# Optimization experiments

Hardware: AMD Instinct MI355X
Metric: run time of the kernel (lower is better)

## Reference

```python
import jax, jax.numpy as jnp
import numpy as np


def _knn(coords, k):
    # coords: [N, 3]. Returns indices of the k nearest neighbors (self excluded): [N, k]
    sq = jnp.sum(coords * coords, axis=1)
    d2 = sq[:, None] + sq[None, :] - 2.0 * (coords @ coords.T)  # [N, N]
    n = coords.shape[0]
    d2 = jnp.where(jnp.eye(n, dtype=bool), jnp.inf, d2)  # loop=False: no self edges
    _, idx = jax.lax.top_k(-d2, k)
    return idx


def setup_inputs() -> dict:
    key = jax.random.key(0)
    ks = jax.random.split(key, 7)
    B, N, C = 8, 4096, 6
    feats = jax.random.normal(ks[0], (B, N, C), dtype=jnp.float32)
    # Glorot-ish scaled weights; PyG GCNConv lin has no bias, bias added post-aggregation.
    W1 = jax.random.normal(ks[1], (6, 64), dtype=jnp.float32) * (1.0 / np.sqrt(6))
    b1 = jnp.zeros((64,), dtype=jnp.float32)
    W2 = jax.random.normal(ks[2], (64, 128), dtype=jnp.float32) * (1.0 / np.sqrt(64))
    b2 = jnp.zeros((128,), dtype=jnp.float32)
    Wf = jax.random.normal(ks[3], (128, 128), dtype=jnp.float32) * (1.0 / np.sqrt(128))
    bf = jnp.zeros((128,), dtype=jnp.float32)
    return {"feats": feats, "W1": W1, "b1": b1, "W2": W2, "b2": b2,
            "Wf": Wf, "bf": bf, "k": 16}


def reference(feats, W1, b1, W2, b2, Wf, bf, k):
    # feats: [B, N, C]; coords = first 3 channels.
    coords = feats[..., :3]
    nbr = jax.vmap(lambda c: _knn(c, k))(coords)  # [B, N, k]
    inv_deg = 1.0 / (k + 1)  # every node has exactly k in-edges + self loop (uniform sym norm)
    x = feats
    for W, b in ((W1, b1), (W2, b2)):
        h = x @ W  # [B, N, H]
        nb = jax.vmap(lambda hb, ib: hb[ib])(h, nbr)  # gather neighbor feats: [B, N, k, H]
        x = jax.nn.relu((nb.sum(axis=2) + h) * inv_deg + b)  # GCN aggregate + bias + ReLU
    return x @ Wf + bf  # [B, N, out_dim]
```

## Files before the change

### kernel.cpp

```cpp
#include <hip/hip_runtime.h>
#include <cstdint>
#include <cstddef>

#define NPTS 4096
#define KNN  16
#define INV_DEG (1.0f / 17.0f)
#define CAP  48
#define TS   512

typedef unsigned long long u64;
typedef unsigned int u32;
typedef float v2f __attribute__((ext_vector_type(2)));

__device__ __forceinline__ u32 mapmono(float f) {
  u32 u = __float_as_uint(f);
  return u ^ ((u32)((int)u >> 31) | 0x80000000u);
}
__device__ __forceinline__ float unmapmono(u32 m) {
  u32 u = (m & 0x80000000u) ? (m ^ 0x80000000u) : ~m;
  return __uint_as_float(u);
}

__global__ __launch_bounds__(512) void knn_kernel(const float* __restrict__ feats,
                                                  int* __restrict__ nbr) {
#pragma clang fp contract(off)
  __shared__ float4 sc[TS];
  __shared__ u64 sbuf[8][2][64];

  const int b = blockIdx.x >> 8;
  const int pbase = (blockIdx.x & 255) * 16;
  const float* fb = feats + (size_t)b * NPTS * 6;
  const int wave = threadIdx.x >> 6;
  const int lane = threadIdx.x & 63;

  int ip[2];
  float xi[2], yi[2], zi[2], sqi[2], tau[2];
  u64 slot[2];
  int cnt[2];
#pragma unroll
  for (int p = 0; p < 2; ++p) {
    ip[p] = pbase + wave * 2 + p;
    const float* fr = fb + (size_t)ip[p] * 6;
    xi[p] = fr[0]; yi[p] = fr[1]; zi[p] = fr[2];
    sqi[p] = __fadd_rn(__fadd_rn(__fmul_rn(xi[p], xi[p]), __fmul_rn(yi[p], yi[p])),
                       __fmul_rn(zi[p], zi[p]));
    tau[p] = __uint_as_float(0x7f800000u);
    slot[p] = ~0ull;
    cnt[p] = 0;
  }

  auto flush = [&](int p, bool fin) {
    u64* wb = &sbuf[wave][p][0];
    if (lane >= cnt[p] && lane < CAP) wb[lane] = ~0ull;
    if (lane < KNN) wb[CAP + lane] = slot[p];
    u64 myk = wb[lane];
    if ((u32)myk == (u32)ip[p]) {
      myk = ~0ull;
      wb[lane] = ~0ull;
    }
    int rank = 0;
#pragma unroll
    for (int m = 0; m < 64; m += 4) {
      u64 k0 = wb[m], k1 = wb[m + 1], k2 = wb[m + 2], k3 = wb[m + 3];
      rank += (int)(k0 < myk) + (int)(k1 < myk) + (int)(k2 < myk) + (int)(k3 < myk);
    }
    if (fin) {
      if (rank < KNN)
        nbr[((size_t)(b * NPTS) + ip[p]) * KNN + rank] = (int)(u32)myk;
    } else {
      if (rank < KNN) wb[rank] = myk;
      u64 s15 = wb[15];
      if (lane < KNN) slot[p] = wb[lane];
      tau[p] = unmapmono((u32)(s15 >> 32));
    }
    cnt[p] = 0;
  };

  for (int tb = 0; tb < NPTS; tb += TS) {
    __syncthreads();
    for (int t = threadIdx.x; t < TS; t += 512) {
      const float* fr = fb + (size_t)(tb + t) * 6;
      const float x = fr[0], y = fr[1], z = fr[2];
      const float sq = __fadd_rn(__fadd_rn(__fmul_rn(x, x), __fmul_rn(y, y)),
                                 __fmul_rn(z, z));
      float4 c; c.x = x; c.y = y; c.z = z; c.w = sq;
      sc[t] = c;
    }
    __syncthreads();

    for (int jb0 = 0; jb0 < TS; jb0 += 64) {
      const int tl = jb0 + lane;
      const int j = tb + tl;
      const float4 c = sc[tl];
      const v2f cx2 = {c.x, c.x}, cy2 = {c.y, c.y}, cz2 = {c.z, c.z},
                sq2 = {c.w, c.w};
      v2f X = {xi[0], xi[1]};
      v2f Y = {yi[0], yi[1]};
      v2f Z = {zi[0], zi[1]};
      v2f SQ = {sqi[0], sqi[1]};
      v2f dot = X * cx2;
      dot = __builtin_elementwise_fma(Y, cy2, dot);
      dot = __builtin_elementwise_fma(Z, cz2, dot);
      v2f two = {2.0f, 2.0f};
      v2f d2v = (SQ + sq2) - two * dot;
      float d2s[2] = {d2v.x, d2v.y};
#pragma unroll
      for (int p = 0; p < 2; ++p) {
        const bool pred = d2s[p] <= tau[p];
        const u64 bal = __ballot(pred);
        if (bal) {
          const int npass = __popcll(bal);
          if (cnt[p] + npass > CAP) flush(p, false);
          const int pos = cnt[p] + (int)__builtin_amdgcn_mbcnt_hi(
                                        (u32)(bal >> 32),
                                        __builtin_amdgcn_mbcnt_lo((u32)bal, 0));
          const u64 key = ((u64)mapmono(d2s[p]) << 32) | (u32)j;
          if (npass <= CAP) {
            if (pred) sbuf[wave][p][pos] = key;
            cnt[p] += npass;
          } else {
            if (pred && pos < CAP) sbuf[wave][p][pos] = key;
            cnt[p] = CAP;
            flush(p, false);
            if (pred && pos >= CAP) sbuf[wave][p][pos - CAP] = key;
            cnt[p] = npass - CAP;
          }
        }
      }
    }
  }
#pragma unroll
  for (int p = 0; p < 2; ++p) flush(p, true);
}

__global__ __launch_bounds__(256) void enc1_kernel(const float* __restrict__ feats,
                                                   const int* __restrict__ nbr,
                                                   const float* __restrict__ W1,
                                                   const float* __restrict__ b1,
                                                   float* __restrict__ x1) {
  __shared__ float af[64][6];
  const int tid = threadIdx.x;
  const int n0 = blockIdx.x * 64;
  const int gb = n0 & ~(NPTS - 1);

  if (tid < 128) {
    const int p = tid >> 1, h = tid & 1;
    const int n = n0 + p;
    const int d0 = h * 3;
    const int* nb = nbr + (size_t)n * KNN;
    const float* fr = feats + (size_t)n * 6 + d0;
    float a0 = fr[0], a1 = fr[1], a2 = fr[2];
#pragma unroll
    for (int t = 0; t < KNN; ++t) {
      const float* fq = feats + (size_t)(gb + nb[t]) * 6 + d0;
      a0 += fq[0]; a1 += fq[1]; a2 += fq[2];
    }
    af[p][d0] = a0; af[p][d0 + 1] = a1; af[p][d0 + 2] = a2;
  }
  __syncthreads();

  const int c = tid & 63, pg = tid >> 6;
  float w[6];
#pragma unroll
  for (int k = 0; k < 6; ++k) w[k] = W1[k * 64 + c];
  const float bv = b1[c];
  for (int pi = 0; pi < 16; ++pi) {
    const int p = pg * 16 + pi;
    float s = 0.f;
#pragma unroll
    for (int k = 0; k < 6; ++k) s = fmaf(af[p][k], w[k], s);
    x1[(size_t)(n0 + p) * 64 + c] = fmaxf(fmaf(s, INV_DEG, bv), 0.f);
  }
}

__global__ __launch_bounds__(256) void enc2_kernel(const float* __restrict__ x1,
                                                   const int* __restrict__ nbr,
                                                   const float* __restrict__ W2,
                                                   const float* __restrict__ b2,
                                                   float* __restrict__ x2) {
  __shared__ float a1s[16][64];
  __shared__ v2f w2s[64][64];
  const int tid = threadIdx.x;
  const int n0 = blockIdx.x * 16;
  const int gb = n0 & ~(NPTS - 1);

#pragma unroll
  for (int i = 0; i < 16; ++i) {
    const int e = tid + 256 * i;
    const int k = e >> 6, l = e & 63;
    v2f w;
    w.x = W2[k * 128 + l];
    w.y = W2[k * 128 + 64 + l];
    w2s[k][l] = w;
  }
  {
    const int p = tid >> 4, c4 = tid & 15;
    const int n = n0 + p;
    const int* nb = nbr + (size_t)n * KNN;
    float4 s = ((const float4*)(x1 + (size_t)n * 64))[c4];
#pragma unroll
    for (int t = 0; t < KNN; ++t) {
      float4 v = ((const float4*)(x1 + (size_t)(gb + nb[t]) * 64))[c4];
      s.x += v.x; s.y += v.y; s.z += v.z; s.w += v.w;
    }
    *((float4*)&a1s[p][c4 * 4]) = s;
  }
  __syncthreads();

  const int wave = tid >> 6, lane = tid & 63;
  const int p0 = wave * 4;
  const float bx = b2[lane], by = b2[lane + 64];
  v2f acc0 = {0, 0}, acc1 = {0, 0}, acc2 = {0, 0}, acc3 = {0, 0};
  for (int k = 0; k < 64; k += 4) {
    const float4 a0 = *(const float4*)&a1s[p0 + 0][k];
    const float4 a1v = *(const float4*)&a1s[p0 + 1][k];
    const float4 a2v = *(const float4*)&a1s[p0 + 2][k];
    const float4 a3v = *(const float4*)&a1s[p0 + 3][k];
#pragma unroll
    for (int kk = 0; kk < 4; ++kk) {
      const v2f w = w2s[k + kk][lane];
      const float e0 = kk == 0 ? a0.x : kk == 1 ? a0.y : kk == 2 ? a0.z : a0.w;
      const float e1 = kk == 0 ? a1v.x : kk == 1 ? a1v.y : kk == 2 ? a1v.z : a1v.w;
      const float e2 = kk == 0 ? a2v.x : kk == 1 ? a2v.y : kk == 2 ? a2v.z : a2v.w;
      const float e3 = kk == 0 ? a3v.x : kk == 1 ? a3v.y : kk == 2 ? a3v.z : a3v.w;
      v2f v0 = {e0, e0}, v1 = {e1, e1}, v2 = {e2, e2}, v3 = {e3, e3};
      acc0 = __builtin_elementwise_fma(v0, w, acc0);
      acc1 = __builtin_elementwise_fma(v1, w, acc1);
      acc2 = __builtin_elementwise_fma(v2, w, acc2);
      acc3 = __builtin_elementwise_fma(v3, w, acc3);
    }
  }
  v2f accs[4] = {acc0, acc1, acc2, acc3};
#pragma unroll
  for (int pi = 0; pi < 4; ++pi) {
    float* row = x2 + (size_t)(n0 + p0 + pi) * 128;
    row[lane] = fmaxf(fmaf(accs[pi].x, INV_DEG, bx), 0.f);
    row[lane + 64] = fmaxf(fmaf(accs[pi].y, INV_DEG, by), 0.f);
  }
}

__global__ __launch_bounds__(256) void enc3_kernel(const float* __restrict__ x2,
                                                   const float* __restrict__ Wf,
                                                   const float* __restrict__ bf,
                                                   float* __restrict__ out) {
  __shared__ float xs[16 * 128];
  __shared__ float part[2][16][128];
  const int tid = threadIdx.x;
  const int n0 = blockIdx.x * 16;

#pragma unroll
  for (int i = 0; i < 2; ++i) {
    const int e = tid + 256 * i;
    ((float4*)xs)[e] = ((const float4*)(x2 + (size_t)n0 * 128))[e];
  }

  const int wave = tid >> 6, lane = tid & 63;
  const int kh = wave & 1, pg = wave >> 1;
  v2f w[64];
#pragma unroll
  for (int j = 0; j < 64; ++j) {
    const int k = kh * 64 + j;
    w[j].x = Wf[k * 128 + lane];
    w[j].y = Wf[k * 128 + 64 + lane];
  }
  __syncthreads();

  for (int pi = 0; pi < 8; ++pi) {
    const int p = pg * 8 + pi;
    v2f acc = {0, 0};
    for (int j = 0; j < 64; j += 4) {
      const float4 a = *(const float4*)&xs[p * 128 + kh * 64 + j];
#pragma unroll
      for (int jj = 0; jj < 4; ++jj) {
        const float e = jj == 0 ? a.x : jj == 1 ? a.y : jj == 2 ? a.z : a.w;
        v2f v = {e, e};
        acc = __builtin_elementwise_fma(v, w[j + jj], acc);
      }
    }
    part[kh][p][lane] = acc.x;
    part[kh][p][lane + 64] = acc.y;
  }
  __syncthreads();

#pragma unroll
  for (int i = 0; i < 8; ++i) {
    const int e = tid + 256 * i;
    const int p = e >> 7, c = e & 127;
    out[(size_t)(n0 + p) * 128 + c] = part[0][p][c] + part[1][p][c] + bf[c];
  }
}

extern "C" void kernel_launch(void* const* d_in, const int* in_sizes, int n_in,
                              void* d_out, int out_size, void* d_ws, size_t ws_size,
                              hipStream_t stream) {
  const float* feats = (const float*)d_in[0];
  const float* W1 = (const float*)d_in[1];
  const float* b1 = (const float*)d_in[2];
  const float* W2 = (const float*)d_in[3];
  const float* b2 = (const float*)d_in[4];
  const float* Wf = (const float*)d_in[5];
  const float* bf = (const float*)d_in[6];
  float* out = (float*)d_out;

  char* ws = (char*)d_ws;
  int* nbr = (int*)ws;
  float* x1 = (float*)(ws + (size_t)(2 << 20));
  float* x2 = out;

  knn_kernel<<<2048, 512, 0, stream>>>(feats, nbr);
  enc1_kernel<<<512, 256, 0, stream>>>(feats, nbr, W1, b1, x1);
  enc2_kernel<<<2048, 256, 0, stream>>>(x1, nbr, W2, b2, x2);
  enc3_kernel<<<2048, 256, 0, stream>>>(x2, Wf, bf, out);
}
```

Baseline: 233.6 us.

## Fuse first GCN layer into KNN kernel and defer key mapping to flush

The first GCN aggregation and its small matmul move into the tail of the KNN kernel. Each wave gathers its 16 neighbours plus itself from the final sorted slot list, sums them in shared memory and writes x1 directly, so the separate enc1 launch and its re-read of nbr go away. The monotone float-to-key mapping and the self-exclusion check leave the per-candidate hot loop and run only at flush time, using a raw-bit sentinel. enc2 and enc3 now process 32 points per block instead of 16, which halves their grids and gives enc2 more accumulators per wave, at the cost of more registers and shared memory.

```diff
diff --git a/kernel.cpp b/kernel.cpp
--- a/kernel.cpp
+++ b/kernel.cpp
@@ -12,17 +12,18 @@
 typedef unsigned int u32;
 typedef float v2f __attribute__((ext_vector_type(2)));
 
-__device__ __forceinline__ u32 mapmono(float f) {
-  u32 u = __float_as_uint(f);
-  return u ^ ((u32)((int)u >> 31) | 0x80000000u);
-}
+#define RAWSENT 0x7F800000FFFFFFFFull
+
 __device__ __forceinline__ float unmapmono(u32 m) {
   u32 u = (m & 0x80000000u) ? (m ^ 0x80000000u) : ~m;
   return __uint_as_float(u);
 }
 
 __global__ __launch_bounds__(512) void knn_kernel(const float* __restrict__ feats,
-                                                  int* __restrict__ nbr) {
+                                                  const float* __restrict__ W1,
+                                                  const float* __restrict__ b1,
+                                                  int* __restrict__ nbr,
+                                                  float* __restrict__ x1) {
 #pragma clang fp contract(off)
   __shared__ float4 sc[TS];
   __shared__ u64 sbuf[8][2][64];
@@ -49,14 +50,17 @@
     cnt[p] = 0;
   }
 
-  auto flush = [&](int p, bool fin) {
+  auto flush = [&](int p) {
     u64* wb = &sbuf[wave][p][0];
-    if (lane >= cnt[p] && lane < CAP) wb[lane] = ~0ull;
+    if (lane >= cnt[p] && lane < CAP) wb[lane] = RAWSENT;
     if (lane < KNN) wb[CAP + lane] = slot[p];
     u64 myk = wb[lane];
-    if ((u32)myk == (u32)ip[p]) {
-      myk = ~0ull;
-      wb[lane] = ~0ull;
+    if (lane < CAP) {
+      u32 hi = (u32)(myk >> 32);
+      hi ^= ((u32)((int)hi >> 31) | 0x80000000u);
+      myk = ((u64)hi << 32) | (u32)myk;
+      if ((u32)myk == (u32)ip[p]) myk = ~0ull;
+      wb[lane] = myk;
     }
     int rank = 0;
 #pragma unroll
@@ -64,15 +68,10 @@
       u64 k0 = wb[m], k1 = wb[m + 1], k2 = wb[m + 2], k3 = wb[m + 3];
       rank += (int)(k0 < myk) + (int)(k1 < myk) + (int)(k2 < myk) + (int)(k3 < myk);
     }
-    if (fin) {
-      if (rank < KNN)
-        nbr[((size_t)(b * NPTS) + ip[p]) * KNN + rank] = (int)(u32)myk;
-    } else {
-      if (rank < KNN) wb[rank] = myk;
-      u64 s15 = wb[15];
-      if (lane < KNN) slot[p] = wb[lane];
-      tau[p] = unmapmono((u32)(s15 >> 32));
-    }
+    if (rank < KNN) wb[rank] = myk;
+    u64 s15 = wb[15];
+    if (lane < KNN) slot[p] = wb[lane];
+    tau[p] = unmapmono((u32)(s15 >> 32));
     cnt[p] = 0;
   };
 
@@ -110,18 +109,18 @@
         const u64 bal = __ballot(pred);
         if (bal) {
           const int npass = __popcll(bal);
-          if (cnt[p] + npass > CAP) flush(p, false);
+          if (cnt[p] + npass > CAP) flush(p);
           const int pos = cnt[p] + (int)__builtin_amdgcn_mbcnt_hi(
                                         (u32)(bal >> 32),
                                         __builtin_amdgcn_mbcnt_lo((u32)bal, 0));
-          const u64 key = ((u64)mapmono(d2s[p]) << 32) | (u32)j;
+          const u64 key = ((u64)__float_as_uint(d2s[p]) << 32) | (u32)j;
           if (npass <= CAP) {
             if (pred) sbuf[wave][p][pos] = key;
             cnt[p] += npass;
           } else {
             if (pred && pos < CAP) sbuf[wave][p][pos] = key;
             cnt[p] = CAP;
-            flush(p, false);
+            flush(p);
             if (pred && pos >= CAP) sbuf[wave][p][pos - CAP] = key;
             cnt[p] = npass - CAP;
           }
@@ -130,46 +129,42 @@
     }
   }
 #pragma unroll
-  for (int p = 0; p < 2; ++p) flush(p, true);
-}
-
-__global__ __launch_bounds__(256) void enc1_kernel(const float* __restrict__ feats,
-                                                   const int* __restrict__ nbr,
-                                                   const float* __restrict__ W1,
-                                                   const float* __restrict__ b1,
-                                                   float* __restrict__ x1) {
-  __shared__ float af[64][6];
-  const int tid = threadIdx.x;
-  const int n0 = blockIdx.x * 64;
-  const int gb = n0 & ~(NPTS - 1);
-
-  if (tid < 128) {
-    const int p = tid >> 1, h = tid & 1;
-    const int n = n0 + p;
-    const int d0 = h * 3;
-    const int* nb = nbr + (size_t)n * KNN;
-    const float* fr = feats + (size_t)n * 6 + d0;
-    float a0 = fr[0], a1 = fr[1], a2 = fr[2];
-#pragma unroll
-    for (int t = 0; t < KNN; ++t) {
-      const float* fq = feats + (size_t)(gb + nb[t]) * 6 + d0;
-      a0 += fq[0]; a1 += fq[1]; a2 += fq[2];
-    }
-    af[p][d0] = a0; af[p][d0 + 1] = a1; af[p][d0 + 2] = a2;
-  }
-  __syncthreads();
-
-  const int c = tid & 63, pg = tid >> 6;
-  float w[6];
-#pragma unroll
-  for (int k = 0; k < 6; ++k) w[k] = W1[k * 64 + c];
-  const float bv = b1[c];
-  for (int pi = 0; pi < 16; ++pi) {
-    const int p = pg * 16 + pi;
+  for (int p = 0; p < 2; ++p) flush(p);
+
+  float* fsc = (float*)&sbuf[wave][0][0];
+  float w1r[6];
+#pragma unroll
+  for (int k = 0; k < 6; ++k) w1r[k] = W1[k * 64 + lane];
+  const float b1r = b1[lane];
+
+#pragma unroll
+  for (int p = 0; p < 2; ++p) {
+    const int n = b * NPTS + ip[p];
+    const int row = (lane < KNN) ? (int)(u32)slot[p] : ip[p];
+    if (lane < KNN)
+      nbr[(size_t)n * KNN + lane] = row;
+    if (lane < 17) {
+      const float* fr = fb + (size_t)row * 6;
+      float2 r0 = *(const float2*)(fr);
+      float2 r1 = *(const float2*)(fr + 2);
+      float2 r2 = *(const float2*)(fr + 4);
+      fsc[lane * 6 + 0] = r0.x; fsc[lane * 6 + 1] = r0.y;
+      fsc[lane * 6 + 2] = r1.x; fsc[lane * 6 + 3] = r1.y;
+      fsc[lane * 6 + 4] = r2.x; fsc[lane * 6 + 5] = r2.y;
+    }
+    __syncthreads();
+    if (lane < 6) {
+      float s = 0.f;
+#pragma unroll
+      for (int t = 0; t < 17; ++t) s += fsc[t * 6 + lane];
+      fsc[102 + lane] = s;
+    }
+    __syncthreads();
     float s = 0.f;
 #pragma unroll
-    for (int k = 0; k < 6; ++k) s = fmaf(af[p][k], w[k], s);
-    x1[(size_t)(n0 + p) * 64 + c] = fmaxf(fmaf(s, INV_DEG, bv), 0.f);
+    for (int k = 0; k < 6; ++k) s = fmaf(fsc[102 + k], w1r[k], s);
+    x1[(size_t)n * 64 + lane] = fmaxf(fmaf(s, INV_DEG, b1r), 0.f);
+    __syncthreads();
   }
 }
 
@@ -178,10 +173,10 @@
                                                    const float* __restrict__ W2,
                                                    const float* __restrict__ b2,
                                                    float* __restrict__ x2) {
-  __shared__ float a1s[16][64];
+  __shared__ float a1s[32][64];
   __shared__ v2f w2s[64][64];
   const int tid = threadIdx.x;
-  const int n0 = blockIdx.x * 16;
+  const int n0 = blockIdx.x * 32;
   const int gb = n0 & ~(NPTS - 1);
 
 #pragma unroll
@@ -193,8 +188,9 @@
     w.y = W2[k * 128 + 64 + l];
     w2s[k][l] = w;
   }
-  {
-    const int p = tid >> 4, c4 = tid & 15;
+#pragma unroll
+  for (int r = 0; r < 2; ++r) {
+    const int p = r * 16 + (tid >> 4), c4 = tid & 15;
     const int n = n0 + p;
     const int* nb = nbr + (size_t)n * KNN;
     float4 s = ((const float4*)(x1 + (size_t)n * 64))[c4];
@@ -208,34 +204,32 @@
   __syncthreads();
 
   const int wave = tid >> 6, lane = tid & 63;
-  const int p0 = wave * 4;
+  const int p0 = wave * 8;
   const float bx = b2[lane], by = b2[lane + 64];
-  v2f acc0 = {0, 0}, acc1 = {0, 0}, acc2 = {0, 0}, acc3 = {0, 0};
+  v2f acc[8];
+#pragma unroll
+  for (int i = 0; i < 8; ++i) acc[i] = (v2f){0, 0};
   for (int k = 0; k < 64; k += 4) {
-    const float4 a0 = *(const float4*)&a1s[p0 + 0][k];
-    const float4 a1v = *(const float4*)&a1s[p0 + 1][k];
-    const float4 a2v = *(const float4*)&a1s[p0 + 2][k];
-    const float4 a3v = *(const float4*)&a1s[p0 + 3][k];
+    float4 a[8];
+#pragma unroll
+    for (int i = 0; i < 8; ++i) a[i] = *(const float4*)&a1s[p0 + i][k];
 #pragma unroll
     for (int kk = 0; kk < 4; ++kk) {
       const v2f w = w2s[k + kk][lane];
-      const float e0 = kk == 0 ? a0.x : kk == 1 ? a0.y : kk == 2 ? a0.z : a0.w;
-      const float e1 = kk == 0 ? a1v.x : kk == 1 ? a1v.y : kk == 2 ? a1v.z : a1v.w;
-      const float e2 = kk == 0 ? a2v.x : kk == 1 ? a2v.y : kk == 2 ? a2v.z : a2v.w;
-      const float e3 = kk == 0 ? a3v.x : kk == 1 ? a3v.y : kk == 2 ? a3v.z : a3v.w;
-      v2f v0 = {e0, e0}, v1 = {e1, e1}, v2 = {e2, e2}, v3 = {e3, e3};
-      acc0 = __builtin_elementwise_fma(v0, w, acc0);
-      acc1 = __builtin_elementwise_fma(v1, w, acc1);
-      acc2 = __builtin_elementwise_fma(v2, w, acc2);
-      acc3 = __builtin_elementwise_fma(v3, w, acc3);
-    }
-  }
-  v2f accs[4] = {acc0, acc1, acc2, acc3};
-#pragma unroll
-  for (int pi = 0; pi < 4; ++pi) {
+#pragma unroll
+      for (int i = 0; i < 8; ++i) {
+        const float e = kk == 0 ? a[i].x : kk == 1 ? a[i].y : kk == 2 ? a[i].z
+                                                                      : a[i].w;
+        v2f v = {e, e};
+        acc[i] = __builtin_elementwise_fma(v, w, acc[i]);
+      }
+    }
+  }
+#pragma unroll
+  for (int pi = 0; pi < 8; ++pi) {
     float* row = x2 + (size_t)(n0 + p0 + pi) * 128;
-    row[lane] = fmaxf(fmaf(accs[pi].x, INV_DEG, bx), 0.f);
-    row[lane + 64] = fmaxf(fmaf(accs[pi].y, INV_DEG, by), 0.f);
+    row[lane] = fmaxf(fmaf(acc[pi].x, INV_DEG, bx), 0.f);
+    row[lane + 64] = fmaxf(fmaf(acc[pi].y, INV_DEG, by), 0.f);
   }
 }
 
@@ -243,13 +237,13 @@
                                                    const float* __restrict__ Wf,
                                                    const float* __restrict__ bf,
                                                    float* __restrict__ out) {
-  __shared__ float xs[16 * 128];
-  __shared__ float part[2][16][128];
+  __shared__ float xs[32 * 128];
+  __shared__ float part[2][32][128];
   const int tid = threadIdx.x;
-  const int n0 = blockIdx.x * 16;
-
-#pragma unroll
-  for (int i = 0; i < 2; ++i) {
+  const int n0 = blockIdx.x * 32;
+
+#pragma unroll
+  for (int i = 0; i < 4; ++i) {
     const int e = tid + 256 * i;
     ((float4*)xs)[e] = ((const float4*)(x2 + (size_t)n0 * 128))[e];
   }
@@ -265,8 +259,8 @@
   }
   __syncthreads();
 
-  for (int pi = 0; pi < 8; ++pi) {
-    const int p = pg * 8 + pi;
+  for (int pi = 0; pi < 16; ++pi) {
+    const int p = pg * 16 + pi;
     v2f acc = {0, 0};
     for (int j = 0; j < 64; j += 4) {
       const float4 a = *(const float4*)&xs[p * 128 + kh * 64 + j];
@@ -283,7 +277,7 @@
   __syncthreads();
 
 #pragma unroll
-  for (int i = 0; i < 8; ++i) {
+  for (int i = 0; i < 16; ++i) {
     const int e = tid + 256 * i;
     const int p = e >> 7, c = e & 127;
     out[(size_t)(n0 + p) * 128 + c] = part[0][p][c] + part[1][p][c] + bf[c];
@@ -307,8 +301,7 @@
   float* x1 = (float*)(ws + (size_t)(2 << 20));
   float* x2 = out;
 
-  knn_kernel<<<2048, 512, 0, stream>>>(feats, nbr);
-  enc1_kernel<<<512, 256, 0, stream>>>(feats, nbr, W1, b1, x1);
-  enc2_kernel<<<2048, 256, 0, stream>>>(x1, nbr, W2, b2, x2);
-  enc3_kernel<<<2048, 256, 0, stream>>>(x2, Wf, bf, out);
-}
+  knn_kernel<<<2048, 512, 0, stream>>>(feats, W1, b1, nbr, x1);
+  enc2_kernel<<<1024, 256, 0, stream>>>(x1, nbr, W2, b2, x2);
+  enc3_kernel<<<1024, 256, 0, stream>>>(x2, Wf, bf, out);
+}
```

New measurement: 232.4 us. About the same (-0.5%).
